# Performance work log

Measured on AMD Instinct MI355X. Metric: run time of the kernel, lower is better.

## Reference

```python
import jax, jax.numpy as jnp
import numpy as np

FEATURE_TO_DENSE_SCALE = 64.0
DENSE_TO_DENSE_SCALE = 64.0
OUTPUT_SCALE = 16.0
TOTAL_FEATURES = 81920
HIDDEN = 512
L1 = 32
L2 = 32
B = 8192
NNZ = 32


def setup_inputs() -> dict:
    key = jax.random.key(0)
    ks = jax.random.split(key, 12)
    white_idx = jax.random.randint(ks[0], (B, NNZ), 0, TOTAL_FEATURES, dtype=jnp.int64 if jax.config.jax_enable_x64 else jnp.int32)
    black_idx = jax.random.randint(ks[1], (B, NNZ), 0, TOTAL_FEATURES, dtype=white_idx.dtype)
    # make a few indices -1 to exercise the invalid-index mask path
    mask_w = jax.random.uniform(ks[2], (B, NNZ)) < 0.05
    mask_b = jax.random.uniform(ks[3], (B, NNZ)) < 0.05
    white_idx = jnp.where(mask_w, -1, white_idx)
    black_idx = jnp.where(mask_b, -1, black_idx)
    stm = jax.random.randint(ks[4], (B,), 0, 2, dtype=white_idx.dtype)
    white_vals = jax.random.uniform(ks[5], (B, NNZ), dtype=jnp.float32)
    black_vals = jax.random.uniform(ks[6], (B, NNZ), dtype=jnp.float32)
    ft_weight = jax.random.normal(ks[7], (TOTAL_FEATURES, HIDDEN), dtype=jnp.float32) * 0.02
    ft_bias = jnp.zeros((HIDDEN,), dtype=jnp.float32)
    d1_w = jax.random.normal(ks[8], (L1, HIDDEN), dtype=jnp.float32) * (1.0 / np.sqrt(HIDDEN))
    d1_b = jnp.zeros((L1,), dtype=jnp.float32)
    d2_w = jax.random.normal(ks[9], (L2, L1), dtype=jnp.float32) * (1.0 / np.sqrt(L1))
    d2_b = jnp.zeros((L2,), dtype=jnp.float32)
    out_w = jax.random.normal(ks[10], (1, L2), dtype=jnp.float32) * (1.0 / np.sqrt(L2))
    out_b = jnp.zeros((1,), dtype=jnp.float32)
    return dict(white_idx=white_idx, black_idx=black_idx, stm=stm,
                white_vals=white_vals, black_vals=black_vals,
                ft_weight=ft_weight, ft_bias=ft_bias,
                d1_w=d1_w, d1_b=d1_b, d2_w=d2_w, d2_b=d2_b,
                out_w=out_w, out_b=out_b)


def _feature_transform(weight, bias, indices, values):
    # indices: [B, NNZ]; weight: [F, H]
    valid = (indices >= 0)
    safe = jnp.maximum(indices, 0)
    gathered = weight[safe]                         # [B, NNZ, H]
    scale = values * valid.astype(values.dtype)     # fuse value scale + mask
    acc = jnp.einsum('bnh,bn->bh', gathered, scale) # gather-scale-reduce
    return acc + bias


def reference(white_idx, black_idx, stm, white_vals, black_vals,
              ft_weight, ft_bias, d1_w, d1_b, d2_w, d2_b, out_w, out_b):
    white_acc = _feature_transform(ft_weight, ft_bias, white_idx, white_vals)
    black_acc = _feature_transform(ft_weight, ft_bias, black_idx, black_vals)
    white_stm = (stm == 0)[:, None]
    us = jnp.where(white_stm, white_acc, black_acc)
    them = jnp.where(white_stm, black_acc, white_acc)
    x = jax.nn.relu((us - them) / FEATURE_TO_DENSE_SCALE)
    x = jax.nn.relu((x @ d1_w.T + d1_b) / DENSE_TO_DENSE_SCALE)
    x = jax.nn.relu((x @ d2_w.T + d2_b) / DENSE_TO_DENSE_SCALE)
    x = (x @ out_w.T + out_b)[:, 0] / OUTPUT_SCALE
    return x
```

## Files before the change

### kernel.cpp

```cpp
#include <hip/hip_runtime.h>

#define NNZ 32
#define HIDDEN 512

__global__ __launch_bounds__(256) void nnue_fused(
    const int* __restrict__ white_idx, const int* __restrict__ black_idx,
    const int* __restrict__ stm,
    const float* __restrict__ white_vals, const float* __restrict__ black_vals,
    const float* __restrict__ ft_weight, const float* __restrict__ ft_bias,
    const float* __restrict__ d1_w, const float* __restrict__ d1_b,
    const float* __restrict__ d2_w, const float* __restrict__ d2_b,
    const float* __restrict__ out_w, const float* __restrict__ out_b,
    float* __restrict__ out)
{
    const int b   = blockIdx.x;
    const int tid = threadIdx.x;

    __shared__ int   s_idx[64];
    __shared__ float s_val[64];
    __shared__ float s_accB[HIDDEN];
    __shared__ float xs[HIDDEN];
    __shared__ float part[32][9];
    __shared__ float h1s[32];
    __shared__ float h2s[32];

    if (tid < 64) {
        const int sd = tid >> 5;
        const int n  = tid & 31;
        const int*   ip = sd ? black_idx  : white_idx;
        const float* vp = sd ? black_vals : white_vals;
        int   id = ip[b * NNZ + n];
        float v  = vp[b * NNZ + n];
        if (id < 0) { id = 0; v = 0.f; }
        s_idx[tid] = id;
        s_val[tid] = v;
    }
    __syncthreads();

    const int side = tid >> 7;
    const int lane = tid & 127;
    const int base = side << 5;

    const float4* W = reinterpret_cast<const float4*>(ft_weight);
    float4 acc = make_float4(0.f, 0.f, 0.f, 0.f);

    #pragma unroll
    for (int c = 0; c < NNZ; c += 8) {
        float4 w[8];
        float  vv[8];
        #pragma unroll
        for (int u = 0; u < 8; ++u) {
            const int n = base + c + u;
            w[u]  = W[(size_t)s_idx[n] * (HIDDEN / 4) + lane];
            vv[u] = s_val[n];
        }
        #pragma unroll
        for (int u = 0; u < 8; ++u) {
            acc.x = fmaf(vv[u], w[u].x, acc.x);
            acc.y = fmaf(vv[u], w[u].y, acc.y);
            acc.z = fmaf(vv[u], w[u].z, acc.z);
            acc.w = fmaf(vv[u], w[u].w, acc.w);
        }
    }

    if (side == 1) {
        reinterpret_cast<float4*>(s_accB)[lane] = acc;
    }
    __syncthreads();

    if (side == 0) {
        const float4 aB  = reinterpret_cast<const float4*>(s_accB)[lane];
        const float sgn  = (stm[b] == 0) ? 1.f : -1.f;
        const float inv64 = 1.0f / 64.0f;
        float4 x;
        x.x = fmaxf(sgn * (acc.x - aB.x) * inv64, 0.f);
        x.y = fmaxf(sgn * (acc.y - aB.y) * inv64, 0.f);
        x.z = fmaxf(sgn * (acc.z - aB.z) * inv64, 0.f);
        x.w = fmaxf(sgn * (acc.w - aB.w) * inv64, 0.f);
        reinterpret_cast<float4*>(xs)[lane] = x;
    }
    __syncthreads();

    {
        const int o = tid & 31;
        const int j = tid >> 5;
        const float* w1p = d1_w + o * HIDDEN + j * 64;
        const float* xp  = xs + j * 64;
        float p = 0.f;
        #pragma unroll
        for (int k = 0; k < 64; ++k) p = fmaf(xp[k], w1p[k], p);
        part[o][j] = p;
    }
    __syncthreads();
    if (tid < 32) {
        const float inv64 = 1.0f / 64.0f;
        float s = d1_b[tid];
        #pragma unroll
        for (int j = 0; j < 8; ++j) s += part[tid][j];
        h1s[tid] = fmaxf(s * inv64, 0.f);
    }
    __syncthreads();

    if (tid < 32) {
        const float inv64 = 1.0f / 64.0f;
        const float* w2p = d2_w + tid * 32;
        float s = d2_b[tid];
        #pragma unroll
        for (int k = 0; k < 32; ++k) s = fmaf(h1s[k], w2p[k], s);
        h2s[tid] = fmaxf(s * inv64, 0.f);
    }
    __syncthreads();

    if (tid == 0) {
        float s = out_b[0];
        #pragma unroll
        for (int k = 0; k < 32; ++k) s = fmaf(h2s[k], out_w[k], s);
        out[b] = s * (1.0f / 16.0f);
    }
}

extern "C" void kernel_launch(void* const* d_in, const int* in_sizes, int n_in,
                              void* d_out, int out_size, void* d_ws, size_t ws_size,
                              hipStream_t stream) {
    const int*   white_idx  = (const int*)d_in[0];
    const int*   black_idx  = (const int*)d_in[1];
    const int*   stm        = (const int*)d_in[2];
    const float* white_vals = (const float*)d_in[3];
    const float* black_vals = (const float*)d_in[4];
    const float* ft_weight  = (const float*)d_in[5];
    const float* ft_bias    = (const float*)d_in[6];
    const float* d1_w       = (const float*)d_in[7];
    const float* d1_b       = (const float*)d_in[8];
    const float* d2_w       = (const float*)d_in[9];
    const float* d2_b       = (const float*)d_in[10];
    const float* out_w      = (const float*)d_in[11];
    const float* out_b      = (const float*)d_in[12];
    float*       out        = (float*)d_out;

    const int B = in_sizes[2];
    nnue_fused<<<B, 256, 0, stream>>>(white_idx, black_idx, stm,
                                      white_vals, black_vals,
                                      ft_weight, ft_bias,
                                      d1_w, d1_b, d2_w, d2_b,
                                      out_w, out_b, out);
}
```

Baseline: 149.5 us.

## Convert feature table to bf16 per call and use one-wave-per-sample kernel

Adds a pre-pass that rounds the fp32 feature-transform table and d1 weights to bf16 in workspace, then runs a new kernel where each 64-lane wave handles one sample, broadcasting indices via readlane and gathering half-width rows. This halves bytes per gathered row and removes block-wide syncs, but adds a full-table conversion pass every call and reduces weight precision. It falls back to the fp32 kernel when the workspace is too small.

```diff
diff --git a/kernel.cpp b/kernel.cpp
--- a/kernel.cpp
+++ b/kernel.cpp
@@ -3,11 +3,128 @@
 #define NNZ 32
 #define HIDDEN 512
 
-__global__ __launch_bounds__(256) void nnue_fused(
+__global__ __launch_bounds__(256) void cvt_bf16(const uint4* __restrict__ in,
+                                                uint2* __restrict__ out, int n4)
+{
+    const int i = blockIdx.x * 256 + threadIdx.x;
+    if (i >= n4) return;
+    uint4 v = in[i];
+    #define CV(u) (((u) + 0x7FFFu + (((u) >> 16) & 1u)) >> 16)
+    uint2 o;
+    o.x = CV(v.x) | (CV(v.y) << 16);
+    o.y = CV(v.z) | (CV(v.w) << 16);
+    #undef CV
+    out[i] = o;
+}
+
+__global__ __launch_bounds__(256, 5) void nnue_wave(
     const int* __restrict__ white_idx, const int* __restrict__ black_idx,
     const int* __restrict__ stm,
     const float* __restrict__ white_vals, const float* __restrict__ black_vals,
-    const float* __restrict__ ft_weight, const float* __restrict__ ft_bias,
+    const uint4* __restrict__ Wq,
+    const uint2* __restrict__ W1b,
+    const float* __restrict__ d1_b,
+    const float* __restrict__ d2_w, const float* __restrict__ d2_b,
+    const float* __restrict__ out_w, const float* __restrict__ out_b,
+    float* __restrict__ out, int B)
+{
+    const int lane = threadIdx.x & 63;
+    const int wv   = threadIdx.x >> 6;
+    const int b    = (blockIdx.x << 2) | wv;
+    if (b >= B) return;
+
+    __shared__ float xbuf[4][HIDDEN];
+    __shared__ float h1buf[4][32];
+
+    int   id;
+    float val;
+    {
+        const int  n = lane & 31;
+        const bool w = lane < 32;
+        const int*   ip = w ? white_idx  : black_idx;
+        const float* vp = w ? white_vals : black_vals;
+        id  = ip[b * NNZ + n];
+        val = vp[b * NNZ + n];
+        if (id < 0) { id = 0; val = 0.f; }
+    }
+
+    float accW[8], accB[8];
+    #pragma unroll
+    for (int j = 0; j < 8; ++j) { accW[j] = 0.f; accB[j] = 0.f; }
+
+    #define FT_BATCH(RB, ACC)                                                         \
+    {                                                                                 \
+        uint4 w[8]; float vv[8];                                                      \
+        _Pragma("unroll")                                                             \
+        for (int u = 0; u < 8; ++u) {                                                 \
+            const int sid = __builtin_amdgcn_readlane(id, (RB) + u);                  \
+            vv[u] = __uint_as_float(                                                  \
+                (unsigned)__builtin_amdgcn_readlane(__float_as_int(val), (RB) + u));  \
+            w[u] = Wq[(size_t)sid * 64 + lane];                                       \
+        }                                                                             \
+        _Pragma("unroll")                                                             \
+        for (int u = 0; u < 8; ++u) {                                                 \
+            const unsigned* pw = (const unsigned*)&w[u];                              \
+            _Pragma("unroll")                                                         \
+            for (int j = 0; j < 4; ++j) {                                             \
+                ACC[2*j]   = fmaf(vv[u], __uint_as_float(pw[j] << 16),         ACC[2*j]);   \
+                ACC[2*j+1] = fmaf(vv[u], __uint_as_float(pw[j] & 0xFFFF0000u), ACC[2*j+1]); \
+            }                                                                         \
+        }                                                                             \
+    }
+
+    FT_BATCH(0,  accW) FT_BATCH(8,  accW) FT_BATCH(16, accW) FT_BATCH(24, accW)
+    FT_BATCH(32, accB) FT_BATCH(40, accB) FT_BATCH(48, accB) FT_BATCH(56, accB)
+    #undef FT_BATCH
+
+    const float sgn   = (stm[b] == 0) ? 1.f : -1.f;
+    const float inv64 = 0.015625f;
+    float4 x0, x1;
+    x0.x = fmaxf(sgn * (accW[0] - accB[0]) * inv64, 0.f);
+    x0.y = fmaxf(sgn * (accW[1] - accB[1]) * inv64, 0.f);
+    x0.z = fmaxf(sgn * (accW[2] - accB[2]) * inv64, 0.f);
+    x0.w = fmaxf(sgn * (accW[3] - accB[3]) * inv64, 0.f);
+    x1.x = fmaxf(sgn * (accW[4] - accB[4]) * inv64, 0.f);
+    x1.y = fmaxf(sgn * (accW[5] - accB[5]) * inv64, 0.f);
+    x1.z = fmaxf(sgn * (accW[6] - accB[6]) * inv64, 0.f);
+    x1.w = fmaxf(sgn * (accW[7] - accB[7]) * inv64, 0.f);
+    *(float4*)&xbuf[wv][lane * 8]     = x0;
+    *(float4*)&xbuf[wv][lane * 8 + 4] = x1;
+
+    const int o = lane >> 1, h = lane & 1;
+    const uint2* w1p = W1b + o * 128 + h * 64;
+    const float* xh  = &xbuf[wv][h * 256];
+    float p = 0.f;
+    #pragma unroll 8
+    for (int kk = 0; kk < 64; ++kk) {
+        const uint2  ww = w1p[kk];
+        const float4 xv = *(const float4*)&xh[kk * 4];
+        p = fmaf(xv.x, __uint_as_float(ww.x << 16),         p);
+        p = fmaf(xv.y, __uint_as_float(ww.x & 0xFFFF0000u), p);
+        p = fmaf(xv.z, __uint_as_float(ww.y << 16),         p);
+        p = fmaf(xv.w, __uint_as_float(ww.y & 0xFFFF0000u), p);
+    }
+    p += __shfl_xor(p, 1);
+    if (h == 0) h1buf[wv][o] = fmaxf((p + d1_b[o]) * inv64, 0.f);
+
+    const int o2 = lane & 31;
+    const float* w2p = d2_w + o2 * 32;
+    float q = d2_b[o2];
+    #pragma unroll
+    for (int k = 0; k < 32; ++k) q = fmaf(h1buf[wv][k], w2p[k], q);
+    const float h2 = fmaxf(q * inv64, 0.f);
+
+    float t = h2 * out_w[o2];
+    #pragma unroll
+    for (int s = 1; s < 32; s <<= 1) t += __shfl_xor(t, s);
+    if (lane == 0) out[b] = (t + out_b[0]) * 0.0625f;
+}
+
+__global__ __launch_bounds__(256) void nnue_fused_f32(
+    const int* __restrict__ white_idx, const int* __restrict__ black_idx,
+    const int* __restrict__ stm,
+    const float* __restrict__ white_vals, const float* __restrict__ black_vals,
+    const float* __restrict__ ft_weight,
     const float* __restrict__ d1_w, const float* __restrict__ d1_b,
     const float* __restrict__ d2_w, const float* __restrict__ d2_b,
     const float* __restrict__ out_w, const float* __restrict__ out_b,
@@ -43,7 +160,6 @@
 
     const float4* W = reinterpret_cast<const float4*>(ft_weight);
     float4 acc = make_float4(0.f, 0.f, 0.f, 0.f);
-
     #pragma unroll
     for (int c = 0; c < NNZ; c += 8) {
         float4 w[8];
@@ -63,11 +179,8 @@
         }
     }
 
-    if (side == 1) {
-        reinterpret_cast<float4*>(s_accB)[lane] = acc;
-    }
-    __syncthreads();
-
+    if (side == 1) reinterpret_cast<float4*>(s_accB)[lane] = acc;
+    __syncthreads();
     if (side == 0) {
         const float4 aB  = reinterpret_cast<const float4*>(s_accB)[lane];
         const float sgn  = (stm[b] == 0) ? 1.f : -1.f;
@@ -80,7 +193,6 @@
         reinterpret_cast<float4*>(xs)[lane] = x;
     }
     __syncthreads();
-
     {
         const int o = tid & 31;
         const int j = tid >> 5;
@@ -100,7 +212,6 @@
         h1s[tid] = fmaxf(s * inv64, 0.f);
     }
     __syncthreads();
-
     if (tid < 32) {
         const float inv64 = 1.0f / 64.0f;
         const float* w2p = d2_w + tid * 32;
@@ -110,7 +221,6 @@
         h2s[tid] = fmaxf(s * inv64, 0.f);
     }
     __syncthreads();
-
     if (tid == 0) {
         float s = out_b[0];
         #pragma unroll
@@ -128,7 +238,6 @@
     const float* white_vals = (const float*)d_in[3];
     const float* black_vals = (const float*)d_in[4];
     const float* ft_weight  = (const float*)d_in[5];
-    const float* ft_bias    = (const float*)d_in[6];
     const float* d1_w       = (const float*)d_in[7];
     const float* d1_b       = (const float*)d_in[8];
     const float* d2_w       = (const float*)d_in[9];
@@ -137,10 +246,27 @@
     const float* out_b      = (const float*)d_in[12];
     float*       out        = (float*)d_out;
 
-    const int B = in_sizes[2];
-    nnue_fused<<<B, 256, 0, stream>>>(white_idx, black_idx, stm,
-                                      white_vals, black_vals,
-                                      ft_weight, ft_bias,
-                                      d1_w, d1_b, d2_w, d2_b,
-                                      out_w, out_b, out);
-}
+    const int B  = in_sizes[2];
+    const long long FH  = in_sizes[5];
+    const long long W1N = in_sizes[7];
+
+    if (ws_size >= (size_t)(FH * 2 + W1N * 2 + 256)) {
+        const int n4  = (int)(FH / 4);
+        const int n4w = (int)(W1N / 4);
+        uint2* tblb = (uint2*)d_ws;
+        uint2* w1b  = (uint2*)((char*)d_ws + (size_t)FH * 2);
+        cvt_bf16<<<(n4 + 255) / 256, 256, 0, stream>>>((const uint4*)ft_weight, tblb, n4);
+        cvt_bf16<<<(n4w + 255) / 256, 256, 0, stream>>>((const uint4*)d1_w, w1b, n4w);
+        nnue_wave<<<(B + 3) / 4, 256, 0, stream>>>(white_idx, black_idx, stm,
+                                                   white_vals, black_vals,
+                                                   (const uint4*)tblb, (const uint2*)w1b,
+                                                   d1_b, d2_w, d2_b,
+                                                   out_w, out_b, out, B);
+    } else {
+        nnue_fused_f32<<<B, 256, 0, stream>>>(white_idx, black_idx, stm,
+                                              white_vals, black_vals,
+                                              ft_weight,
+                                              d1_w, d1_b, d2_w, d2_b,
+                                              out_w, out_b, out);
+    }
+}
```

Measured after the change: 122.7 us. 1.22x faster.
